# Performance work log

Hardware: AMD Instinct MI355X
Metric: run time of the kernel (lower is better)

## Reference

```python
import jax, jax.numpy as jnp
import numpy as np

N = 24000; E = 384000; NT = 3; IN = 128; HID = 32; ED = 64; NE = 5; FFN = 64; C = 16
HEADS = (8, 8, 1); ALPHA = 0.05; DAL = 2


def _lrelu(x, s):
    return jnp.where(x >= 0, x, s * x)


def _elu(x):
    return jnp.where(x > 0, x, jnp.expm1(x))


def _ln(x, g, b, eps=1e-5):
    m = x.mean(-1, keepdims=True)
    v = ((x - m) ** 2).mean(-1, keepdims=True)
    return (x - m) / jnp.sqrt(v + eps) * g + b


def _l2n(x, eps=1e-12):
    return x / jnp.maximum(jnp.linalg.norm(x, axis=1, keepdims=True), eps)


def _ta(h, src, dst, e_feat, edge_emb, W, We, al, ar, ae, bias, res_W, res_attn, act):
    # SimpleHGN-style heterogeneous graph attention layer (TALayer)
    Hh = al.shape[0]
    feat = (h @ W).reshape(N, Hh, HID)                       # [N,H,D]
    ee = (edge_emb[e_feat] @ We).reshape(E, Hh, ED)          # [E,H,ED]
    el = (feat * al).sum(-1)                                 # [N,H]
    er = (feat * ar).sum(-1)                                 # [N,H]
    lg = _lrelu(el[src] + er[dst] + (ee * ae).sum(-1), 0.2)  # [E,H]
    m = jax.ops.segment_max(lg, dst, num_segments=N)         # edge softmax over dst
    a = jnp.exp(lg - m[dst])
    a = a / jax.ops.segment_sum(a, dst, num_segments=N)[dst]
    if res_attn is not None:
        a = a * (1.0 - ALPHA) + res_attn * ALPHA             # residual attention carry-over
    rst = jax.ops.segment_sum(a[:, :, None] * feat[src], dst, num_segments=N)
    if res_W is not None:
        rst = rst + (h @ res_W).reshape(N, Hh, HID)
    rst = rst + bias
    if act:
        rst = _elu(rst)
    return rst, jax.lax.stop_gradient(a)


def forward(feats, fc_W, fc_b, ntype_emb, W_ntype,
            ta0_edge_emb, ta0_W, ta0_We, ta0_al, ta0_ar, ta0_ae, ta0_bias,
            ta1_edge_emb, ta1_W, ta1_We, ta1_al, ta1_ar, ta1_ae, ta1_bias, ta1_res_W,
            ta2_edge_emb, ta2_W, ta2_We, ta2_al, ta2_ar, ta2_ae, ta2_bias, ta2_res_W,
            da_ln1_g, da_ln1_b, da_Wq, da_bq, da_Wk, da_bk, da_Wv, da_bv, da_Wo, da_bo,
            da_ln2_g, da_ln2_b, da_W1, da_b1, da_W2, da_b2, final_W, logits_W,
            e_feat, node_type, src, dst):
    # per-node-type input projection + leaky_relu(0.01), concat over types -> [N,HID]
    h = _lrelu(jnp.einsum('tni,tio->tno', feats, fc_W) + fc_b[:, None, :], 0.01).reshape(N, HID)
    ntype_feat = (ntype_emb @ W_ntype)[node_type]            # [N,HID]
    h = h * ntype_feat
    h0, a0 = _ta(h, src, dst, e_feat, ta0_edge_emb, ta0_W, ta0_We, ta0_al, ta0_ar, ta0_ae, ta0_bias, None, None, True)
    h = h0.reshape(N, -1)
    h1, _ = _ta(h, src, dst, e_feat, ta1_edge_emb, ta1_W, ta1_We, ta1_al, ta1_ar, ta1_ae, ta1_bias, ta1_res_W, a0, True)
    h = h1.reshape(N, -1)
    hf, _ = _ta(h, src, dst, e_feat, ta2_edge_emb, ta2_W, ta2_We, ta2_al, ta2_ar, ta2_ae, ta2_bias, ta2_res_W, None, False)
    h_feat = hf.reshape(N, HID)
    # dim-wise transformer (DALayer stack): tokens = HID dims, channel = 1
    x = (h_feat * ntype_feat)[:, :, None]                    # [N,HID,1]
    for l in range(DAL):
        y = _ln(x, da_ln1_g[l], da_ln1_b[l])
        q = y @ da_Wq[l] + da_bq[l]
        k = y @ da_Wk[l] + da_bk[l]
        v = y @ da_Wv[l] + da_bv[l]
        att = jax.nn.softmax(jnp.einsum('nqd,nkd->nqk', q, k), axis=-1)  # scale=att_size**-0.5=1
        x = x + (jnp.einsum('nqk,nkd->nqd', att, v) @ da_Wo[l] + da_bo[l])
        y = _ln(x, da_ln2_g[l], da_ln2_b[l])
        x = x + (jax.nn.gelu(y @ da_W1[l] + da_b1[l], approximate=False) @ da_W2[l] + da_b2[l])
    h_dim = _l2n(x[:, :, 0])
    h_final = jnp.concatenate([_l2n(h_feat), h_dim], axis=1) @ final_W
    logits = jax.nn.relu(h_final) @ logits_W
    return logits / jnp.maximum(jnp.linalg.norm(logits, axis=1, keepdims=True), 1e-12)


def setup_inputs():
    key = jax.random.key(0)
    ks = iter(jax.random.split(key, 96))
    def rn(shape, s=0.1):
        return jax.random.normal(next(ks), shape, jnp.float32) * s
    inp = {}
    inp["feats"] = jax.random.normal(next(ks), (NT, N // NT, IN), jnp.float32)
    inp["e_feat"] = jax.random.randint(next(ks), (E,), 0, NE)
    inp["node_type"] = jax.random.randint(next(ks), (N,), 0, NT)
    inp["src"] = jax.random.randint(next(ks), (E,), 0, N)
    inp["dst"] = jax.random.randint(next(ks), (E,), 0, N)
    inp["fc_W"] = rn((NT, IN, HID)); inp["fc_b"] = rn((NT, HID))
    inp["ntype_emb"] = rn((NT, HID)); inp["W_ntype"] = rn((HID, HID))
    ins = (HID, HID * HEADS[0], HID * HEADS[1])
    for l in range(3):
        Hh = HEADS[l]; di = ins[l]; p = "ta%d_" % l
        inp[p + "edge_emb"] = rn((NE, ED))
        inp[p + "W"] = rn((di, Hh * HID))
        inp[p + "We"] = rn((ED, Hh * ED))
        inp[p + "al"] = rn((Hh, HID)); inp[p + "ar"] = rn((Hh, HID)); inp[p + "ae"] = rn((Hh, ED))
        inp[p + "bias"] = jnp.zeros((Hh, HID), jnp.float32)
        if l > 0:
            inp[p + "res_W"] = rn((di, Hh * HID))
    inp["da_ln1_g"] = jnp.ones((DAL, 1), jnp.float32); inp["da_ln1_b"] = jnp.zeros((DAL, 1), jnp.float32)
    inp["da_Wq"] = rn((DAL, 1, 1)); inp["da_bq"] = jnp.zeros((DAL, 1), jnp.float32)
    inp["da_Wk"] = rn((DAL, 1, 1)); inp["da_bk"] = jnp.zeros((DAL, 1), jnp.float32)
    inp["da_Wv"] = rn((DAL, 1, 1)); inp["da_bv"] = jnp.zeros((DAL, 1), jnp.float32)
    inp["da_Wo"] = rn((DAL, 1, 1)); inp["da_bo"] = jnp.zeros((DAL, 1), jnp.float32)
    inp["da_ln2_g"] = jnp.ones((DAL, 1), jnp.float32); inp["da_ln2_b"] = jnp.zeros((DAL, 1), jnp.float32)
    inp["da_W1"] = rn((DAL, 1, FFN)); inp["da_b1"] = jnp.zeros((DAL, FFN), jnp.float32)
    inp["da_W2"] = rn((DAL, FFN, 1)); inp["da_b2"] = jnp.zeros((DAL, 1), jnp.float32)
    inp["final_W"] = rn((2 * HID, HID))
    inp["logits_W"] = rn((HID, C))
    return inp


def reference(feats, fc_W, fc_b, ntype_emb, W_ntype,
              ta0_edge_emb, ta0_W, ta0_We, ta0_al, ta0_ar, ta0_ae, ta0_bias,
              ta1_edge_emb, ta1_W, ta1_We, ta1_al, ta1_ar, ta1_ae, ta1_bias, ta1_res_W,
              ta2_edge_emb, ta2_W, ta2_We, ta2_al, ta2_ar, ta2_ae, ta2_bias, ta2_res_W,
              da_ln1_g, da_ln1_b, da_Wq, da_bq, da_Wk, da_bk, da_Wv, da_bv, da_Wo, da_bo,
              da_ln2_g, da_ln2_b, da_W1, da_b1, da_W2, da_b2, final_W, logits_W,
              e_feat, node_type, src, dst):
    return forward(feats, fc_W, fc_b, ntype_emb, W_ntype,
                   ta0_edge_emb, ta0_W, ta0_We, ta0_al, ta0_ar, ta0_ae, ta0_bias,
                   ta1_edge_emb, ta1_W, ta1_We, ta1_al, ta1_ar, ta1_ae, ta1_bias, ta1_res_W,
                   ta2_edge_emb, ta2_W, ta2_We, ta2_al, ta2_ar, ta2_ae, ta2_bias, ta2_res_W,
                   da_ln1_g, da_ln1_b, da_Wq, da_bq, da_Wk, da_bk, da_Wv, da_bv, da_Wo, da_bo,
                   da_ln2_g, da_ln2_b, da_W1, da_b1, da_W2, da_b2, final_W, logits_W,
                   e_feat, node_type, src, dst)
```

## Files before the change

kernel.cpp:

```cpp
#include <hip/hip_runtime.h>
#include <math.h>

constexpr int kN = 24000;
constexpr int kE = 384000;
constexpr float kAlpha = 0.05f;

typedef unsigned int   u32;
typedef unsigned short u16;
typedef __attribute__((ext_vector_type(8))) short short8;
typedef __attribute__((ext_vector_type(4))) float float4v;

__device__ __forceinline__ float bf2f(u16 x) { return __uint_as_float(((u32)x) << 16); }
__device__ __forceinline__ u16 f2bf(float f) {
  u32 u = __float_as_uint(f);
  return (u16)((u + 0x7fffu + ((u >> 16) & 1u)) >> 16);
}

__global__ void __launch_bounds__(256) zero_ints_kernel(int* __restrict__ p, int n) {
  int i = blockIdx.x * 256 + threadIdx.x;
  if (i < n) p[i] = 0;
}

__global__ void __launch_bounds__(256) count_kernel(const int* __restrict__ dst,
                                                    int* __restrict__ counts) {
  int e = blockIdx.x * 256 + threadIdx.x;
  if (e < kE) atomicAdd(&counts[dst[e]], 1);
}

__global__ void __launch_bounds__(1024) scan_kernel(const int* __restrict__ counts,
                                                    int* __restrict__ row_start) {
  __shared__ int wsum[16];
  __shared__ int carry_s;
  int tid = threadIdx.x, lane = tid & 63, wid = tid >> 6;
  if (tid == 0) { carry_s = 0; row_start[0] = 0; }
  __syncthreads();
  for (int base = 0; base < kN; base += 1024) {
    int x = (base + tid < kN) ? counts[base + tid] : 0;
    #pragma unroll
    for (int off = 1; off < 64; off <<= 1) {
      int y = __shfl_up(x, off);
      if (lane >= off) x += y;
    }
    if (lane == 63) wsum[wid] = x;
    __syncthreads();
    if (tid < 16) {
      int wv = wsum[tid];
      #pragma unroll
      for (int off = 1; off < 16; off <<= 1) {
        int y = __shfl_up(wv, off);
        if (tid >= off) wv += y;
      }
      wsum[tid] = wv;
    }
    __syncthreads();
    int incl = x + carry_s + (wid > 0 ? wsum[wid - 1] : 0);
    if (base + tid < kN) row_start[base + tid + 1] = incl;
    __syncthreads();
    if (tid == 1023) carry_s = incl;
    __syncthreads();
  }
}

__global__ void __launch_bounds__(256) scatter_kernel(const int* __restrict__ dst,
                                                      const int* __restrict__ row_start,
                                                      int* __restrict__ cursor,
                                                      int* __restrict__ edge_ids) {
  int e = blockIdx.x * 256 + threadIdx.x;
  if (e < kE) {
    int n = dst[e];
    int pos = row_start[n] + atomicAdd(&cursor[n], 1);
    edge_ids[pos] = e;
  }
}

__global__ void __launch_bounds__(256) prepack_kernel(
    const float* __restrict__ W0, const float* __restrict__ al0, const float* __restrict__ ar0,
    const float* __restrict__ W1, const float* __restrict__ al1, const float* __restrict__ ar1,
    const float* __restrict__ rW1,
    const float* __restrict__ W2, const float* __restrict__ al2, const float* __restrict__ ar2,
    const float* __restrict__ rW2,
    u16* __restrict__ WT0, u16* __restrict__ WT1, u16* __restrict__ WT2,
    const float* __restrict__ ntype_emb, const float* __restrict__ W_ntype,
    const float* __restrict__ emb0, const float* __restrict__ We0, const float* __restrict__ ae0,
    const float* __restrict__ emb1, const float* __restrict__ We1, const float* __restrict__ ae1,
    const float* __restrict__ emb2, const float* __restrict__ We2, const float* __restrict__ ae2,
    const float* __restrict__ ln1_b, const float* __restrict__ Wv, const float* __restrict__ bv,
    const float* __restrict__ Wo, const float* __restrict__ bo,
    const float* __restrict__ ln2_b, const float* __restrict__ DW1, const float* __restrict__ Db1,
    const float* __restrict__ DW2, const float* __restrict__ Db2,
    float* __restrict__ ntf, float* __restrict__ eterm, float* __restrict__ dadelta) {
  __shared__ float wae[17][64];
  __shared__ float red[128];
  int tid = threadIdx.x;
  if (blockIdx.x < 744) {
    const int SZ0 = 10240, SZ1 = 576 * 256;
    int gid = blockIdx.x * 256 + tid;
    float v = 0.f;
    if (gid < 2048) {
      int n = gid / 32, k = gid % 32;
      if (n < 8)       { for (int d = 0; d < 32; ++d) v += W0[k * 256 + n * 32 + d] * al0[n * 32 + d]; }
      else if (n < 16) { int h = n - 8; for (int d = 0; d < 32; ++d) v += W0[k * 256 + h * 32 + d] * ar0[h * 32 + d]; }
      WT0[n * 32 + k] = f2bf(v);
    } else if (gid < SZ0) {
      int i = gid - 2048;
      int h = i >> 10, rem = i & 1023, d = rem >> 5, k = rem & 31;
      WT0[2048 + i] = f2bf(W0[k * 256 + h * 32 + d]);
    } else if (gid < SZ0 + SZ1) {
      int i = gid - SZ0;
      int n = i / 256, k = i % 256;
      if (n < 256) v = W1[k * 256 + n];
      else if (n < 264) { int h = n - 256; for (int d = 0; d < 32; ++d) v += W1[k * 256 + h * 32 + d] * al1[h * 32 + d]; }
      else if (n < 272) { int h = n - 264; for (int d = 0; d < 32; ++d) v += W1[k * 256 + h * 32 + d] * ar1[h * 32 + d]; }
      else if (n < 528) v = rW1[k * 256 + (n - 272)];
      WT1[n * 256 + k] = f2bf(v);
    } else {
      int i = gid - SZ0 - SZ1;
      int n = i / 256, k = i % 256;
      if (n < 32) v = W2[k * 32 + n];
      else if (n == 32) { for (int d = 0; d < 32; ++d) v += W2[k * 32 + d] * al2[d]; }
      else if (n == 33) { for (int d = 0; d < 32; ++d) v += W2[k * 32 + d] * ar2[d]; }
      else if (n < 66) v = rW2[k * 32 + (n - 34)];
      WT2[n * 256 + k] = f2bf(v);
    }
  } else {
    for (int idx = tid; idx < 17 * 64; idx += 256) {
      int hg = idx >> 6, k = idx & 63;
      const float* We; const float* ae; int Hh, h;
      if (hg < 8)       { We = We0; ae = ae0; Hh = 8; h = hg; }
      else if (hg < 16) { We = We1; ae = ae1; Hh = 8; h = hg - 8; }
      else              { We = We2; ae = ae2; Hh = 1; h = 0; }
      float s = 0.f;
      for (int d = 0; d < 64; ++d) s += We[(size_t)k * Hh * 64 + h * 64 + d] * ae[h * 64 + d];
      wae[hg][k] = s;
    }
    __syncthreads();
    for (int id = tid; id < 85; id += 256) {
      const float* emb; int Hh, t, h, hg, base;
      if (id < 40)      { emb = emb0; Hh = 8; t = id / 8;  h = id % 8; hg = h;      base = 0;  }
      else if (id < 80) { int i = id - 40; emb = emb1; Hh = 8; t = i / 8; h = i % 8; hg = 8 + h; base = 40; }
      else              { int i = id - 80; emb = emb2; Hh = 1; t = i;    h = 0;     hg = 16;    base = 80; }
      float s = 0.f;
      for (int k = 0; k < 64; ++k) s += emb[t * 64 + k] * wae[hg][k];
      eterm[base + t * Hh + h] = s;
    }
    for (int idx = tid; idx < 96; idx += 256) {
      int t = idx / 32, o = idx % 32;
      float s = 0.f;
      for (int k = 0; k < 32; ++k) s += ntype_emb[t * 32 + k] * W_ntype[k * 32 + o];
      ntf[idx] = s;
    }
    for (int i2 = tid; i2 < 128; i2 += 256) {
      int l = i2 >> 6, j = i2 & 63;
      float u = ln2_b[l] * DW1[l * 64 + j] + Db1[l * 64 + j];
      float g = 0.5f * u * (1.0f + erff(u * 0.7071067811865476f));
      red[i2] = g * DW2[l * 64 + j];
    }
    __syncthreads();
    if (tid == 0) {
      float delta = 0.f;
      for (int l = 0; l < 2; ++l) {
        float vs = ln1_b[l] * Wv[l] + bv[l];
        delta += vs * Wo[l] + bo[l] + Db2[l];
      }
      for (int i = 0; i < 128; ++i) delta += red[i];
      *dadelta = delta;
    }
  }
}

__global__ void __launch_bounds__(256) inproj_kernel(
    const float* __restrict__ feats, const float* __restrict__ fc_W,
    const float* __restrict__ fc_b, const float* __restrict__ ntf,
    const int* __restrict__ node_type, u16* __restrict__ hb) {
  int t = blockIdx.x * 256 + threadIdx.x;
  if (t >= kN * 32) return;
  int n = t >> 5, o = t & 31;
  int ty = n / 8000;
  const float* fr = &feats[(size_t)n * 128];
  const float* w  = &fc_W[(size_t)ty * 4096 + o];
  float s = fc_b[ty * 32 + o];
  #pragma unroll
  for (int k = 0; k < 128; k += 4) {
    float4 f = *(const float4*)&fr[k];
    s += f.x * w[(k + 0) * 32] + f.y * w[(k + 1) * 32]
       + f.z * w[(k + 2) * 32] + f.w * w[(k + 3) * 32];
  }
  s = (s < 0.f) ? 0.01f * s : s;
  hb[t] = f2bf(s * ntf[node_type[n] * 32 + o]);
}

template <int K>
__global__ void __launch_bounds__(256) mfma_gemm_kernel(
    const u16* __restrict__ A, const u16* __restrict__ WT,
    const float* __restrict__ bias,
    u16* __restrict__ featb, float* __restrict__ el, float* __restrict__ er,
    u16* __restrict__ resb, float* __restrict__ resf,
    int NT, int N1, int HH, int N2) {
  constexpr int RB = K * 2;
  constexpr int CPR = K / 8;
  __shared__ __align__(16) u16 As[64 * K];
  __shared__ __align__(16) u16 Bs[64 * K];
  const int tid = threadIdx.x;
  const int l = tid & 63;
  const int w = tid >> 6;
  const int wm = w >> 1, wn = w & 1;
  const int m0 = blockIdx.x * 64;
  const int kslot = l >> 4;
  const int l15 = l & 15;

  #pragma unroll
  for (int c = tid; c < 64 * CPR; c += 256) {
    int row = c / CPR, ch = c - row * CPR;
    int off = (row * RB + ch * 16) ^ ((row & 7) << 4);
    *(uint4*)((char*)As + off) = *(const uint4*)(A + (size_t)(m0 + row) * K + ch * 8);
  }

  for (int ct = 0; ct < NT; ++ct) {
    __syncthreads();
    #pragma unroll
    for (int c = tid; c < 64 * CPR; c += 256) {
      int row = c / CPR, ch = c - row * CPR;
      int off = (row * RB + ch * 16) ^ ((row & 7) << 4);
      *(uint4*)((char*)Bs + off) = *(const uint4*)(WT + (size_t)(ct * 64 + row) * K + ch * 8);
    }
    __syncthreads();

    float4v acc[2][2];
    #pragma unroll
    for (int f = 0; f < 2; ++f)
      #pragma unroll
      for (int g = 0; g < 2; ++g) { acc[f][g][0]=0.f; acc[f][g][1]=0.f; acc[f][g][2]=0.f; acc[f][g][3]=0.f; }

    #pragma unroll
    for (int kc = 0; kc < K; kc += 32) {
      short8 af[2], bf[2];
      #pragma unroll
      for (int f = 0; f < 2; ++f) {
        int row = wm * 32 + f * 16 + l15;
        int off = (row * RB + kc * 2 + kslot * 16) ^ ((row & 7) << 4);
        af[f] = *(const short8*)((const char*)As + off);
      }
      #pragma unroll
      for (int g = 0; g < 2; ++g) {
        int n = wn * 32 + g * 16 + l15;
        int off = (n * RB + kc * 2 + kslot * 16) ^ ((n & 7) << 4);
        bf[g] = *(const short8*)((const char*)Bs + off);
      }
      #pragma unroll
      for (int f = 0; f < 2; ++f)
        #pragma unroll
        for (int g = 0; g < 2; ++g)
          acc[f][g] = __builtin_amdgcn_mfma_f32_16x16x32_bf16(af[f], bf[g], acc[f][g], 0, 0, 0);
    }

    const int rbase = kslot * 4;
    #pragma unroll
    for (int f = 0; f < 2; ++f) {
      #pragma unroll
      for (int g = 0; g < 2; ++g) {
        int gc = ct * 64 + wn * 32 + g * 16 + l15;
        #pragma unroll
        for (int reg = 0; reg < 4; ++reg) {
          int gr = m0 + wm * 32 + f * 16 + rbase + reg;
          float v = acc[f][g][reg];
          if (gc < N1) {
            featb[(size_t)gr * N1 + gc] = f2bf(v);
          } else if (gc < N1 + HH) {
            el[(size_t)gr * HH + (gc - N1)] = v;
          } else if (gc < N1 + 2 * HH) {
            er[(size_t)gr * HH + (gc - N1 - HH)] = v;
          } else if (gc < N1 + 2 * HH + N2) {
            int c2 = gc - N1 - 2 * HH;
            float vv = v + bias[c2];
            if (resb) resb[(size_t)gr * N2 + c2] = f2bf(vv);
            else      resf[(size_t)gr * N2 + c2] = vv;
          }
        }
      }
    }
  }
}

__global__ void __launch_bounds__(256) agg8h_kernel(
    const int* __restrict__ row_start, const int* __restrict__ edge_ids,
    const int* __restrict__ src, const int* __restrict__ ef,
    const float* __restrict__ el, const float* __restrict__ er,
    const float* __restrict__ eterm,
    const u16* __restrict__ Hb,
    _Float16* __restrict__ a0h,
    u16* __restrict__ Gb) {
  int n = (blockIdx.x * 256 + threadIdx.x) >> 6;
  if (n >= kN) return;
  int l = threadIdx.x & 63;
  int h = l >> 3, s = l & 7;
  int s0 = row_start[n], s1 = row_start[n + 1];
  float ern = er[n * 8 + h];
  float et0 = eterm[0 * 8 + h], et1 = eterm[1 * 8 + h], et2 = eterm[2 * 8 + h];
  float et3 = eterm[3 * 8 + h], et4 = eterm[4 * 8 + h];
  float m = -1e30f, ssum = 0.f;
  for (int i = s0 + s; i < s1; i += 8) {
    int e = edge_ids[i];
    int efc = ef[e];
    float etv = (efc == 0) ? et0 : (efc == 1) ? et1 : (efc == 2) ? et2 : (efc == 3) ? et3 : et4;
    float lg = el[src[e] * 8 + h] + ern + etv;
    lg = (lg < 0.f) ? 0.2f * lg : lg;
    if (lg > m) { ssum = ssum * expf(m - lg) + 1.f; m = lg; }
    else        { ssum += expf(lg - m); }
  }
  #pragma unroll
  for (int mk = 1; mk <= 4; mk <<= 1) {
    float om = __shfl_xor(m, mk);
    float os = __shfl_xor(ssum, mk);
    float nm = fmaxf(m, om);
    ssum = ssum * expf(m - nm) + os * expf(om - nm);
    m = nm;
  }
  float inv = 1.f / ssum;
  float4 acc = make_float4(0.f, 0.f, 0.f, 0.f);
  int i = s0;
  for (; i + 8 <= s1; i += 8) {
    int e = edge_ids[i + s];
    int sek = src[e];
    int efc = ef[e];
    float etv = (efc == 0) ? et0 : (efc == 1) ? et1 : (efc == 2) ? et2 : (efc == 3) ? et3 : et4;
    float lg = el[sek * 8 + h] + ern + etv;
    lg = (lg < 0.f) ? 0.2f * lg : lg;
    float am = expf(lg - m) * inv;
    a0h[(size_t)e * 8 + h] = (_Float16)am;
    #pragma unroll
    for (int j = 0; j < 8; ++j) {
      float aj = __shfl(am, (h << 3) + j);
      int sej = __shfl(sek, j);
      ushort4 fv = *(const ushort4*)(Hb + (size_t)sej * 32 + s * 4);
      acc.x = fmaf(aj, bf2f(fv.x), acc.x);
      acc.y = fmaf(aj, bf2f(fv.y), acc.y);
      acc.z = fmaf(aj, bf2f(fv.z), acc.z);
      acc.w = fmaf(aj, bf2f(fv.w), acc.w);
    }
  }
  if (i < s1) {
    int cnt = s1 - i;
    float am = 0.f; int sek = 0;
    if (s < cnt) {
      int e = edge_ids[i + s];
      sek = src[e];
      int efc = ef[e];
      float etv = (efc == 0) ? et0 : (efc == 1) ? et1 : (efc == 2) ? et2 : (efc == 3) ? et3 : et4;
      float lg = el[sek * 8 + h] + ern + etv;
      lg = (lg < 0.f) ? 0.2f * lg : lg;
      am = expf(lg - m) * inv;
      a0h[(size_t)e * 8 + h] = (_Float16)am;
    }
    for (int j = 0; j < cnt; ++j) {
      float aj = __shfl(am, (h << 3) + j);
      int sej = __shfl(sek, j);
      ushort4 fv = *(const ushort4*)(Hb + (size_t)sej * 32 + s * 4);
      acc.x = fmaf(aj, bf2f(fv.x), acc.x);
      acc.y = fmaf(aj, bf2f(fv.y), acc.y);
      acc.z = fmaf(aj, bf2f(fv.z), acc.z);
      acc.w = fmaf(aj, bf2f(fv.w), acc.w);
    }
  }
  ushort4 pw;
  pw.x = f2bf(acc.x); pw.y = f2bf(acc.y); pw.z = f2bf(acc.z); pw.w = f2bf(acc.w);
  *(ushort4*)(Gb + (size_t)n * 256 + h * 32 + s * 4) = pw;
}

__global__ void __launch_bounds__(256) bd_gemm_kernel(
    const u16* __restrict__ Gb,
    const u16* __restrict__ WbdT,
    const float* __restrict__ bias,
    u16* __restrict__ outb) {
  __shared__ __align__(16) u16 As[64 * 256];
  __shared__ __align__(16) u16 Bs[8 * 32 * 32];
  const int tid = threadIdx.x;
  const int l = tid & 63;
  const int w = tid >> 6;
  const int m0 = blockIdx.x * 64;
  const int kslot = l >> 4, l15 = l & 15;
  for (int c = tid; c < 64 * 32; c += 256) {
    int row = c >> 5, ch = c & 31;
    int off = (row * 512 + ch * 16) ^ ((row & 7) << 4);
    *(uint4*)((char*)As + off) = *(const uint4*)(Gb + (size_t)(m0 + row) * 256 + ch * 8);
  }
  for (int c = tid; c < 256 * 4; c += 256) {
    int r = c >> 2, ch = c & 3;
    int off = (r * 64 + ch * 16) ^ ((r & 7) << 4);
    *(uint4*)((char*)Bs + off) = *(const uint4*)(WbdT + (size_t)r * 32 + ch * 8);
  }
  __syncthreads();
  #pragma unroll
  for (int hh = 0; hh < 2; ++hh) {
    int h = w * 2 + hh;
    short8 af[4];
    #pragma unroll
    for (int f = 0; f < 4; ++f) {
      int row = f * 16 + l15;
      int off = (row * 512 + h * 64 + kslot * 16) ^ ((row & 7) << 4);
      af[f] = *(const short8*)((const char*)As + off);
    }
    short8 bf[2];
    #pragma unroll
    for (int g = 0; g < 2; ++g) {
      int r = h * 32 + g * 16 + l15;
      int off = (r * 64 + kslot * 16) ^ ((r & 7) << 4);
      bf[g] = *(const short8*)((const char*)Bs + off);
    }
    #pragma unroll
    for (int f = 0; f < 4; ++f) {
      #pragma unroll
      for (int g = 0; g < 2; ++g) {
        float4v acc = {0.f, 0.f, 0.f, 0.f};
        acc = __builtin_amdgcn_mfma_f32_16x16x32_bf16(af[f], bf[g], acc, 0, 0, 0);
        #pragma unroll
        for (int reg = 0; reg < 4; ++reg) {
          int gr = m0 + f * 16 + kslot * 4 + reg;
          int gc = h * 32 + g * 16 + l15;
          float v = acc[reg] + bias[gc];
          v = (v > 0.f) ? v : expm1f(v);
          outb[(size_t)gr * 256 + gc] = f2bf(v);
        }
      }
    }
  }
}

__global__ void __launch_bounds__(256) agg8w_kernel(
    const int* __restrict__ row_start, const int* __restrict__ edge_ids,
    const int* __restrict__ src, const int* __restrict__ ef,
    const float* __restrict__ el, const float* __restrict__ er,
    const float* __restrict__ eterm,
    const u16* __restrict__ featb,
    const _Float16* __restrict__ a0h,
    const u16* __restrict__ accb,
    u16* __restrict__ outb) {
  int n = (blockIdx.x * 256 + threadIdx.x) >> 6;
  if (n >= kN) return;
  int l = threadIdx.x & 63;
  int h = l >> 3, s = l & 7;
  int s0 = row_start[n], s1 = row_start[n + 1];
  float ern = er[n * 8 + h];
  float et0 = eterm[0 * 8 + h], et1 = eterm[1 * 8 + h], et2 = eterm[2 * 8 + h];
  float et3 = eterm[3 * 8 + h], et4 = eterm[4 * 8 + h];
  float m = -1e30f, ssum = 0.f;
  for (int i = s0 + s; i < s1; i += 8) {
    int e = edge_ids[i];
    int efc = ef[e];
    float etv = (efc == 0) ? et0 : (efc == 1) ? et1 : (efc == 2) ? et2 : (efc == 3) ? et3 : et4;
    float lg = el[src[e] * 8 + h] + ern + etv;
    lg = (lg < 0.f) ? 0.2f * lg : lg;
    if (lg > m) { ssum = ssum * expf(m - lg) + 1.f; m = lg; }
    else        { ssum += expf(lg - m); }
  }
  #pragma unroll
  for (int mk = 1; mk <= 4; mk <<= 1) {
    float om = __shfl_xor(m, mk);
    float os = __shfl_xor(ssum, mk);
    float nm = fmaxf(m, om);
    ssum = ssum * expf(m - nm) + os * expf(om - nm);
    m = nm;
  }
  float inv = 1.f / ssum;
  const size_t rowoff = (size_t)n * 256 + h * 32 + s * 4;
  ushort4 rv = *(const ushort4*)(accb + rowoff);
  float4 acc = make_float4(bf2f(rv.x), bf2f(rv.y), bf2f(rv.z), bf2f(rv.w));
  int i = s0;
  for (; i + 8 <= s1; i += 8) {
    int e = edge_ids[i + s];
    int sek = src[e];
    int efc = ef[e];
    float etv = (efc == 0) ? et0 : (efc == 1) ? et1 : (efc == 2) ? et2 : (efc == 3) ? et3 : et4;
    float lg = el[sek * 8 + h] + ern + etv;
    lg = (lg < 0.f) ? 0.2f * lg : lg;
    float am = expf(lg - m) * inv;
    am = am * (1.f - kAlpha) + (float)a0h[(size_t)e * 8 + h] * kAlpha;
    #pragma unroll
    for (int j = 0; j < 8; ++j) {
      float aj = __shfl(am, (h << 3) + j);
      int sej = __shfl(sek, j);
      ushort4 fv = *(const ushort4*)(featb + (size_t)sej * 256 + h * 32 + s * 4);
      acc.x = fmaf(aj, bf2f(fv.x), acc.x);
      acc.y = fmaf(aj, bf2f(fv.y), acc.y);
      acc.z = fmaf(aj, bf2f(fv.z), acc.z);
      acc.w = fmaf(aj, bf2f(fv.w), acc.w);
    }
  }
  if (i < s1) {
    int cnt = s1 - i;
    float am = 0.f; int sek = 0;
    if (s < cnt) {
      int e = edge_ids[i + s];
      sek = src[e];
      int efc = ef[e];
      float etv = (efc == 0) ? et0 : (efc == 1) ? et1 : (efc == 2) ? et2 : (efc == 3) ? et3 : et4;
      float lg = el[sek * 8 + h] + ern + etv;
      lg = (lg < 0.f) ? 0.2f * lg : lg;
      am = expf(lg - m) * inv;
      am = am * (1.f - kAlpha) + (float)a0h[(size_t)e * 8 + h] * kAlpha;
    }
    for (int j = 0; j < cnt; ++j) {
      float aj = __shfl(am, (h << 3) + j);
      int sej = __shfl(sek, j);
      ushort4 fv = *(const ushort4*)(featb + (size_t)sej * 256 + h * 32 + s * 4);
      acc.x = fmaf(aj, bf2f(fv.x), acc.x);
      acc.y = fmaf(aj, bf2f(fv.y), acc.y);
      acc.z = fmaf(aj, bf2f(fv.z), acc.z);
      acc.w = fmaf(aj, bf2f(fv.w), acc.w);
    }
  }
  acc.x = (acc.x > 0.f) ? acc.x : expm1f(acc.x);
  acc.y = (acc.y > 0.f) ? acc.y : expm1f(acc.y);
  acc.z = (acc.z > 0.f) ? acc.z : expm1f(acc.z);
  acc.w = (acc.w > 0.f) ? acc.w : expm1f(acc.w);
  ushort4 pw;
  pw.x = f2bf(acc.x); pw.y = f2bf(acc.y); pw.z = f2bf(acc.z); pw.w = f2bf(acc.w);
  *(ushort4*)(outb + rowoff) = pw;
}

__global__ void __launch_bounds__(256) aggw1_final_kernel(
    const int* __restrict__ row_start, const int* __restrict__ edge_ids,
    const int* __restrict__ src, const int* __restrict__ ef,
    const float* __restrict__ el, const float* __restrict__ er,
    const float* __restrict__ eterm,
    const u16* __restrict__ featb,
    const float* __restrict__ S2,
    const float* __restrict__ ntf, const int* __restrict__ node_type,
    const float* __restrict__ dadelta,
    const float* __restrict__ finalW, const float* __restrict__ logitsW,
    float* __restrict__ out) {
  __shared__ float fWs[2048];
  __shared__ float lWs[512];
  __shared__ float abuf[8][32];
  __shared__ float bbuf[8][32];
  __shared__ float sbuf[8][32];
  const int tid = threadIdx.x;
  for (int i = tid; i < 2048; i += 256) fWs[i] = finalW[i];
  for (int i = tid; i < 512; i += 256) lWs[i] = logitsW[i];
  const int slot = tid >> 5;
  const int g = tid & 31;
  const int gb = tid & 32;
  const int n = blockIdx.x * 8 + slot;
  const int s0 = row_start[n], s1 = row_start[n + 1];
  float ern = er[n];
  float et0 = eterm[0], et1 = eterm[1], et2 = eterm[2], et3 = eterm[3], et4 = eterm[4];
  float m = -1e30f, ssum = 0.f;
  for (int i = s0 + g; i < s1; i += 32) {
    int e = edge_ids[i];
    int efc = ef[e];
    float etv = (efc == 0) ? et0 : (efc == 1) ? et1 : (efc == 2) ? et2 : (efc == 3) ? et3 : et4;
    float lg = el[src[e]] + ern + etv;
    lg = (lg < 0.f) ? 0.2f * lg : lg;
    if (lg > m) { ssum = ssum * expf(m - lg) + 1.f; m = lg; }
    else        { ssum += expf(lg - m); }
  }
  #pragma unroll
  for (int mk = 1; mk <= 16; mk <<= 1) {
    float om = __shfl_xor(m, mk);
    float os = __shfl_xor(ssum, mk);
    float nm = fmaxf(m, om);
    ssum = ssum * expf(m - nm) + os * expf(om - nm);
    m = nm;
  }
  float inv = 1.f / ssum;
  float acc = S2[(size_t)n * 32 + g];
  int i = s0;
  for (; i + 32 <= s1; i += 32) {
    int e = edge_ids[i + g];
    int sek = src[e];
    int efc = ef[e];
    float etv = (efc == 0) ? et0 : (efc == 1) ? et1 : (efc == 2) ? et2 : (efc == 3) ? et3 : et4;
    float lg = el[sek] + ern + etv;
    lg = (lg < 0.f) ? 0.2f * lg : lg;
    float am = expf(lg - m) * inv;
    #pragma unroll
    for (int j = 0; j < 32; ++j) {
      float aj = __shfl(am, gb + j);
      int sej = __shfl(sek, gb + j);
      acc = fmaf(aj, bf2f(featb[(size_t)sej * 32 + g]), acc);
    }
  }
  if (i < s1) {
    int cnt = s1 - i;
    float am = 0.f; int sek = 0;
    if (g < cnt) {
      int e = edge_ids[i + g];
      sek = src[e];
      int efc = ef[e];
      float etv = (efc == 0) ? et0 : (efc == 1) ? et1 : (efc == 2) ? et2 : (efc == 3) ? et3 : et4;
      float lg = el[sek] + ern + etv;
      lg = (lg < 0.f) ? 0.2f * lg : lg;
      am = expf(lg - m) * inv;
    }
    for (int j = 0; j < cnt; ++j) {
      float aj = __shfl(am, gb + j);
      int sej = __shfl(sek, gb + j);
      acc = fmaf(aj, bf2f(featb[(size_t)sej * 32 + g]), acc);
    }
  }
  float delta = dadelta[0];
  float ntv = ntf[node_type[n] * 32 + g];
  float av = acc;
  float bv = acc * ntv + delta;
  float na = av * av, nb = bv * bv;
  #pragma unroll
  for (int mk = 1; mk <= 16; mk <<= 1) {
    na += __shfl_xor(na, mk);
    nb += __shfl_xor(nb, mk);
  }
  float inva = 1.f / fmaxf(sqrtf(na), 1e-12f);
  float invb = 1.f / fmaxf(sqrtf(nb), 1e-12f);
  __syncthreads();
  abuf[slot][g] = av * inva;
  bbuf[slot][g] = bv * invb;
  __syncthreads();
  float s = 0.f;
  #pragma unroll
  for (int d = 0; d < 32; ++d)
    s += abuf[slot][d] * fWs[d * 32 + g] + bbuf[slot][d] * fWs[(32 + d) * 32 + g];
  s = fmaxf(s, 0.f);
  sbuf[slot][g] = s;
  __syncthreads();
  if (g < 16) {
    float lg = 0.f;
    #pragma unroll
    for (int o = 0; o < 32; ++o) lg += sbuf[slot][o] * lWs[o * 16 + g];
    float nl = lg * lg;
    #pragma unroll
    for (int mk = 1; mk <= 8; mk <<= 1) nl += __shfl_xor(nl, mk);
    float invl = 1.f / fmaxf(sqrtf(nl), 1e-12f);
    out[(size_t)n * 16 + g] = lg * invl;
  }
}

extern "C" void kernel_launch(void* const* d_in, const int* in_sizes, int n_in,
                              void* d_out, int out_size, void* d_ws, size_t ws_size,
                              hipStream_t stream) {
  const float* feats     = (const float*)d_in[0];
  const int*   e_feat    = (const int*)d_in[1];
  const int*   node_type = (const int*)d_in[2];
  const int*   src       = (const int*)d_in[3];
  const int*   dst       = (const int*)d_in[4];
  const float* fc_W      = (const float*)d_in[5];
  const float* fc_b      = (const float*)d_in[6];
  const float* ntype_emb = (const float*)d_in[7];
  const float* W_ntype   = (const float*)d_in[8];
  const float* ta_edge_emb[3] = {(const float*)d_in[9],  (const float*)d_in[16], (const float*)d_in[24]};
  const float* ta_W[3]        = {(const float*)d_in[10], (const float*)d_in[17], (const float*)d_in[25]};
  const float* ta_We[3]       = {(const float*)d_in[11], (const float*)d_in[18], (const float*)d_in[26]};
  const float* ta_al[3]       = {(const float*)d_in[12], (const float*)d_in[19], (const float*)d_in[27]};
  const float* ta_ar[3]       = {(const float*)d_in[13], (const float*)d_in[20], (const float*)d_in[28]};
  const float* ta_ae[3]       = {(const float*)d_in[14], (const float*)d_in[21], (const float*)d_in[29]};
  const float* ta_bias[3]     = {(const float*)d_in[15], (const float*)d_in[22], (const float*)d_in[30]};
  const float* ta1_res_W = (const float*)d_in[23];
  const float* ta2_res_W = (const float*)d_in[31];
  const float* da_ln1_b  = (const float*)d_in[33];
  const float* da_Wv     = (const float*)d_in[38];
  const float* da_bv     = (const float*)d_in[39];
  const float* da_Wo     = (const float*)d_in[40];
  const float* da_bo     = (const float*)d_in[41];
  const float* da_ln2_b  = (const float*)d_in[43];
  const float* da_W1     = (const float*)d_in[44];
  const float* da_b1     = (const float*)d_in[45];
  const float* da_W2     = (const float*)d_in[46];
  const float* da_b2     = (const float*)d_in[47];
  const float* final_W   = (const float*)d_in[48];
  const float* logits_W  = (const float*)d_in[49];
  float* out = (float*)d_out;

  char* base = (char*)d_ws;
  int* iws       = (int*)base;
  int* counts    = iws;
  int* cursor    = iws + kN;
  int* row_start = iws + 2 * kN;
  int* edge_ids  = iws + 2 * kN + kN + 1;
  char* p = base + (size_t)456004 * 4;
  float* ntf = (float*)p;                     p += 512;
  float* etm = (float*)p;                     p += 512;
  float* dad = (float*)p;                     p += 64;
  float* el  = (float*)p;                     p += (size_t)kN * 8 * 4;
  float* er  = (float*)p;                     p += (size_t)kN * 8 * 4;
  float* S2  = (float*)p;                     p += (size_t)kN * 32 * 4;
  u16*   Hb  = (u16*)p;                       p += (size_t)kN * 32 * 2;
  _Float16* a0h = (_Float16*)p;               p += (size_t)kE * 8 * 2;
  u16* featb = (u16*)p;                       p += (size_t)kN * 256 * 2;
  u16* Rb0   = (u16*)p;                       p += (size_t)kN * 256 * 2;
  u16* Rpr   = (u16*)p;                       p += (size_t)kN * 256 * 2;
  u16* WT0   = (u16*)p;                       p += (size_t)320 * 32 * 2;
  u16* WT1   = (u16*)p;                       p += (size_t)576 * 256 * 2;
  u16* WT2   = (u16*)p;                       p += (size_t)128 * 256 * 2;
  u16* WT0el = WT0;
  u16* Wbd0T = WT0 + 2048;

  zero_ints_kernel<<<(2 * kN + 255) / 256, 256, 0, stream>>>(counts, 2 * kN);
  count_kernel<<<kE / 256, 256, 0, stream>>>(dst, counts);
  scan_kernel<<<1, 1024, 0, stream>>>(counts, row_start);
  scatter_kernel<<<kE / 256, 256, 0, stream>>>(dst, row_start, cursor, edge_ids);

  prepack_kernel<<<745, 256, 0, stream>>>(
      ta_W[0], ta_al[0], ta_ar[0],
      ta_W[1], ta_al[1], ta_ar[1], ta1_res_W,
      ta_W[2], ta_al[2], ta_ar[2], ta2_res_W,
      WT0, WT1, WT2,
      ntype_emb, W_ntype,
      ta_edge_emb[0], ta_We[0], ta_ae[0],
      ta_edge_emb[1], ta_We[1], ta_ae[1],
      ta_edge_emb[2], ta_We[2], ta_ae[2],
      da_ln1_b, da_Wv, da_bv, da_Wo, da_bo,
      da_ln2_b, da_W1, da_b1, da_W2, da_b2,
      ntf, etm, dad);

  inproj_kernel<<<(kN * 32) / 256, 256, 0, stream>>>(feats, fc_W, fc_b, ntf, node_type, Hb);

  mfma_gemm_kernel<32><<<kN / 64, 256, 0, stream>>>(
      Hb, WT0el, nullptr, nullptr, el, er, nullptr, nullptr, 1, 0, 8, 0);
  agg8h_kernel<<<kN / 4, 256, 0, stream>>>(
      row_start, edge_ids, src, e_feat, el, er, etm, Hb, a0h, featb);
  bd_gemm_kernel<<<kN / 64, 256, 0, stream>>>(featb, Wbd0T, ta_bias[0], Rb0);

  mfma_gemm_kernel<256><<<kN / 64, 256, 0, stream>>>(
      Rb0, WT1, ta_bias[1], featb, el, er, Rpr, nullptr, 9, 256, 8, 256);
  agg8w_kernel<<<kN / 4, 256, 0, stream>>>(
      row_start, edge_ids, src, e_feat, el, er, etm + 40, featb, a0h, Rpr, Rpr);

  mfma_gemm_kernel<256><<<kN / 64, 256, 0, stream>>>(
      Rpr, WT2, ta_bias[2], featb, el, er, nullptr, S2, 2, 32, 1, 32);
  aggw1_final_kernel<<<kN / 8, 256, 0, stream>>>(
      row_start, edge_ids, src, e_feat, el, er, etm + 80, featb, S2,
      ntf, node_type, dad, final_W, logits_W, out);
}
```

Measured before the change: 490.0 us.

## Use head-major slab layouts, split GEMM column tiles across blocks, parallel CSR alloc

```diff
diff --git a/kernel.cpp b/kernel.cpp
--- a/kernel.cpp
+++ b/kernel.cpp
@@ -27,38 +27,23 @@
   if (e < kE) atomicAdd(&counts[dst[e]], 1);
 }
 
-__global__ void __launch_bounds__(1024) scan_kernel(const int* __restrict__ counts,
+__global__ void __launch_bounds__(256) alloc_kernel(const int* __restrict__ counts,
+                                                    int* __restrict__ gcur,
                                                     int* __restrict__ row_start) {
-  __shared__ int wsum[16];
-  __shared__ int carry_s;
-  int tid = threadIdx.x, lane = tid & 63, wid = tid >> 6;
-  if (tid == 0) { carry_s = 0; row_start[0] = 0; }
-  __syncthreads();
-  for (int base = 0; base < kN; base += 1024) {
-    int x = (base + tid < kN) ? counts[base + tid] : 0;
-    #pragma unroll
-    for (int off = 1; off < 64; off <<= 1) {
-      int y = __shfl_up(x, off);
-      if (lane >= off) x += y;
-    }
-    if (lane == 63) wsum[wid] = x;
-    __syncthreads();
-    if (tid < 16) {
-      int wv = wsum[tid];
-      #pragma unroll
-      for (int off = 1; off < 16; off <<= 1) {
-        int y = __shfl_up(wv, off);
-        if (tid >= off) wv += y;
-      }
-      wsum[tid] = wv;
-    }
-    __syncthreads();
-    int incl = x + carry_s + (wid > 0 ? wsum[wid - 1] : 0);
-    if (base + tid < kN) row_start[base + tid + 1] = incl;
-    __syncthreads();
-    if (tid == 1023) carry_s = incl;
-    __syncthreads();
-  }
+  int t = blockIdx.x * 256 + threadIdx.x;
+  int lane = threadIdx.x & 63;
+  int c = (t < kN) ? counts[t] : 0;
+  int x = c;
+  #pragma unroll
+  for (int off = 1; off < 64; off <<= 1) {
+    int y = __shfl_up(x, off);
+    if (lane >= off) x += y;
+  }
+  int wtotal = __shfl(x, 63);
+  int base = 0;
+  if (lane == 63) base = atomicAdd(gcur, wtotal);
+  base = __shfl(base, 63);
+  if (t < kN) row_start[t] = base + x - c;
 }
 
 __global__ void __launch_bounds__(256) scatter_kernel(const int* __restrict__ dst,
@@ -189,13 +174,13 @@
   hb[t] = f2bf(s * ntf[node_type[n] * 32 + o]);
 }
 
-template <int K>
+template <int K, bool SLAB>
 __global__ void __launch_bounds__(256) mfma_gemm_kernel(
     const u16* __restrict__ A, const u16* __restrict__ WT,
     const float* __restrict__ bias,
     u16* __restrict__ featb, float* __restrict__ el, float* __restrict__ er,
     u16* __restrict__ resb, float* __restrict__ resf,
-    int NT, int N1, int HH, int N2) {
+    int tpb, int N1, int HH, int N2) {
   constexpr int RB = K * 2;
   constexpr int CPR = K / 8;
   __shared__ __align__(16) u16 As[64 * K];
@@ -204,7 +189,7 @@
   const int l = tid & 63;
   const int w = tid >> 6;
   const int wm = w >> 1, wn = w & 1;
-  const int m0 = blockIdx.x * 64;
+  const int m0 = blockIdx.y * 64;
   const int kslot = l >> 4;
   const int l15 = l & 15;
 
@@ -215,7 +200,8 @@
     *(uint4*)((char*)As + off) = *(const uint4*)(A + (size_t)(m0 + row) * K + ch * 8);
   }
 
-  for (int ct = 0; ct < NT; ++ct) {
+  for (int t = 0; t < tpb; ++t) {
+    int ct = blockIdx.x * tpb + t;
     __syncthreads();
     #pragma unroll
     for (int c = tid; c < 64 * CPR; c += 256) {
@@ -264,11 +250,14 @@
           int gr = m0 + wm * 32 + f * 16 + rbase + reg;
           float v = acc[f][g][reg];
           if (gc < N1) {
-            featb[(size_t)gr * N1 + gc] = f2bf(v);
+            if (SLAB) featb[((size_t)(gc >> 5) * kN + gr) * 32 + (gc & 31)] = f2bf(v);
+            else      featb[(size_t)gr * N1 + gc] = f2bf(v);
           } else if (gc < N1 + HH) {
-            el[(size_t)gr * HH + (gc - N1)] = v;
+            if (SLAB) el[(size_t)(gc - N1) * kN + gr] = v;
+            else      el[(size_t)gr * HH + (gc - N1)] = v;
           } else if (gc < N1 + 2 * HH) {
-            er[(size_t)gr * HH + (gc - N1 - HH)] = v;
+            if (SLAB) er[(size_t)(gc - N1 - HH) * kN + gr] = v;
+            else      er[(size_t)gr * HH + (gc - N1 - HH)] = v;
           } else if (gc < N1 + 2 * HH + N2) {
             int c2 = gc - N1 - 2 * HH;
             float vv = v + bias[c2];
@@ -282,18 +271,19 @@
 }
 
 __global__ void __launch_bounds__(256) agg8h_kernel(
-    const int* __restrict__ row_start, const int* __restrict__ edge_ids,
+    const int* __restrict__ row_start, const int* __restrict__ counts,
+    const int* __restrict__ edge_ids,
     const int* __restrict__ src, const int* __restrict__ ef,
     const float* __restrict__ el, const float* __restrict__ er,
     const float* __restrict__ eterm,
     const u16* __restrict__ Hb,
-    _Float16* __restrict__ a0h,
+    _Float16* __restrict__ a0s,
     u16* __restrict__ Gb) {
   int n = (blockIdx.x * 256 + threadIdx.x) >> 6;
   if (n >= kN) return;
   int l = threadIdx.x & 63;
   int h = l >> 3, s = l & 7;
-  int s0 = row_start[n], s1 = row_start[n + 1];
+  int s0 = row_start[n], s1 = s0 + counts[n];
   float ern = er[n * 8 + h];
   float et0 = eterm[0 * 8 + h], et1 = eterm[1 * 8 + h], et2 = eterm[2 * 8 + h];
   float et3 = eterm[3 * 8 + h], et4 = eterm[4 * 8 + h];
@@ -326,7 +316,7 @@
     float lg = el[sek * 8 + h] + ern + etv;
     lg = (lg < 0.f) ? 0.2f * lg : lg;
     float am = expf(lg - m) * inv;
-    a0h[(size_t)e * 8 + h] = (_Float16)am;
+    a0s[(size_t)h * kE + e] = (_Float16)am;
     #pragma unroll
     for (int j = 0; j < 8; ++j) {
       float aj = __shfl(am, (h << 3) + j);
@@ -349,7 +339,7 @@
       float lg = el[sek * 8 + h] + ern + etv;
       lg = (lg < 0.f) ? 0.2f * lg : lg;
       am = expf(lg - m) * inv;
-      a0h[(size_t)e * 8 + h] = (_Float16)am;
+      a0s[(size_t)h * kE + e] = (_Float16)am;
     }
     for (int j = 0; j < cnt; ++j) {
       float aj = __shfl(am, (h << 3) + j);
@@ -367,10 +357,8 @@
 }
 
 __global__ void __launch_bounds__(256) bd_gemm_kernel(
-    const u16* __restrict__ Gb,
-    const u16* __restrict__ WbdT,
-    const float* __restrict__ bias,
-    u16* __restrict__ outb) {
+    const u16* __restrict__ Gb, const u16* __restrict__ WbdT,
+    const float* __restrict__ bias, u16* __restrict__ outb) {
   __shared__ __align__(16) u16 As[64 * 256];
   __shared__ __align__(16) u16 Bs[8 * 32 * 32];
   const int tid = threadIdx.x;
@@ -425,29 +413,37 @@
   }
 }
 
-__global__ void __launch_bounds__(256) agg8w_kernel(
-    const int* __restrict__ row_start, const int* __restrict__ edge_ids,
+__global__ void __launch_bounds__(256) agg8s_kernel(
+    const int* __restrict__ row_start, const int* __restrict__ counts,
+    const int* __restrict__ edge_ids,
     const int* __restrict__ src, const int* __restrict__ ef,
-    const float* __restrict__ el, const float* __restrict__ er,
+    const float* __restrict__ el_s,
+    const float* __restrict__ er_s,
     const float* __restrict__ eterm,
-    const u16* __restrict__ featb,
-    const _Float16* __restrict__ a0h,
+    const u16* __restrict__ feat_s,
+    const _Float16* __restrict__ a0s,
     const u16* __restrict__ accb,
     u16* __restrict__ outb) {
-  int n = (blockIdx.x * 256 + threadIdx.x) >> 6;
-  if (n >= kN) return;
-  int l = threadIdx.x & 63;
-  int h = l >> 3, s = l & 7;
-  int s0 = row_start[n], s1 = row_start[n + 1];
-  float ern = er[n * 8 + h];
-  float et0 = eterm[0 * 8 + h], et1 = eterm[1 * 8 + h], et2 = eterm[2 * 8 + h];
-  float et3 = eterm[3 * 8 + h], et4 = eterm[4 * 8 + h];
+  const int hd = blockIdx.x & 7;
+  const int chunk = blockIdx.x >> 3;
+  const int tid = threadIdx.x;
+  const int slot = tid >> 3;
+  const int g = tid & 7;
+  const int n = chunk * 32 + slot;
+  const int lbase = (tid & 63) & ~7;
+  int s0 = row_start[n], s1 = s0 + counts[n];
+  const float* el_h = el_s + (size_t)hd * kN;
+  const u16* feat_h = feat_s + (size_t)hd * kN * 32;
+  const _Float16* a0_h = a0s + (size_t)hd * kE;
+  float ern = er_s[(size_t)hd * kN + n];
+  float et0 = eterm[0 * 8 + hd], et1 = eterm[1 * 8 + hd], et2 = eterm[2 * 8 + hd];
+  float et3 = eterm[3 * 8 + hd], et4 = eterm[4 * 8 + hd];
   float m = -1e30f, ssum = 0.f;
-  for (int i = s0 + s; i < s1; i += 8) {
+  for (int i = s0 + g; i < s1; i += 8) {
     int e = edge_ids[i];
     int efc = ef[e];
     float etv = (efc == 0) ? et0 : (efc == 1) ? et1 : (efc == 2) ? et2 : (efc == 3) ? et3 : et4;
-    float lg = el[src[e] * 8 + h] + ern + etv;
+    float lg = el_h[src[e]] + ern + etv;
     lg = (lg < 0.f) ? 0.2f * lg : lg;
     if (lg > m) { ssum = ssum * expf(m - lg) + 1.f; m = lg; }
     else        { ssum += expf(lg - m); }
@@ -461,24 +457,24 @@
     m = nm;
   }
   float inv = 1.f / ssum;
-  const size_t rowoff = (size_t)n * 256 + h * 32 + s * 4;
+  const size_t rowoff = (size_t)n * 256 + hd * 32 + g * 4;
   ushort4 rv = *(const ushort4*)(accb + rowoff);
   float4 acc = make_float4(bf2f(rv.x), bf2f(rv.y), bf2f(rv.z), bf2f(rv.w));
   int i = s0;
   for (; i + 8 <= s1; i += 8) {
-    int e = edge_ids[i + s];
+    int e = edge_ids[i + g];
     int sek = src[e];
     int efc = ef[e];
     float etv = (efc == 0) ? et0 : (efc == 1) ? et1 : (efc == 2) ? et2 : (efc == 3) ? et3 : et4;
-    float lg = el[sek * 8 + h] + ern + etv;
+    float lg = el_h[sek] + ern + etv;
     lg = (lg < 0.f) ? 0.2f * lg : lg;
     float am = expf(lg - m) * inv;
-    am = am * (1.f - kAlpha) + (float)a0h[(size_t)e * 8 + h] * kAlpha;
+    am = am * (1.f - kAlpha) + (float)a0_h[e] * kAlpha;
     #pragma unroll
     for (int j = 0; j < 8; ++j) {
-      float aj = __shfl(am, (h << 3) + j);
-      int sej = __shfl(sek, j);
-      ushort4 fv = *(const ushort4*)(featb + (size_t)sej * 256 + h * 32 + s * 4);
+      float aj = __shfl(am, lbase + j);
+      int sej = __shfl(sek, lbase + j);
+      ushort4 fv = *(const ushort4*)(feat_h + (size_t)sej * 32 + g * 4);
       acc.x = fmaf(aj, bf2f(fv.x), acc.x);
       acc.y = fmaf(aj, bf2f(fv.y), acc.y);
       acc.z = fmaf(aj, bf2f(fv.z), acc.z);
@@ -488,20 +484,20 @@
   if (i < s1) {
     int cnt = s1 - i;
     float am = 0.f; int sek = 0;
-    if (s < cnt) {
-      int e = edge_ids[i + s];
+    if (g < cnt) {
+      int e = edge_ids[i + g];
       sek = src[e];
       int efc = ef[e];
       float etv = (efc == 0) ? et0 : (efc == 1) ? et1 : (efc == 2) ? et2 : (efc == 3) ? et3 : et4;
-      float lg = el[sek * 8 + h] + ern + etv;
+      float lg = el_h[sek] + ern + etv;
       lg = (lg < 0.f) ? 0.2f * lg : lg;
       am = expf(lg - m) * inv;
-      am = am * (1.f - kAlpha) + (float)a0h[(size_t)e * 8 + h] * kAlpha;
+      am = am * (1.f - kAlpha) + (float)a0_h[e] * kAlpha;
     }
     for (int j = 0; j < cnt; ++j) {
-      float aj = __shfl(am, (h << 3) + j);
-      int sej = __shfl(sek, j);
-      ushort4 fv = *(const ushort4*)(featb + (size_t)sej * 256 + h * 32 + s * 4);
+      float aj = __shfl(am, lbase + j);
+      int sej = __shfl(sek, lbase + j);
+      ushort4 fv = *(const ushort4*)(feat_h + (size_t)sej * 32 + g * 4);
       acc.x = fmaf(aj, bf2f(fv.x), acc.x);
       acc.y = fmaf(aj, bf2f(fv.y), acc.y);
       acc.z = fmaf(aj, bf2f(fv.z), acc.z);
@@ -518,7 +514,8 @@
 }
 
 __global__ void __launch_bounds__(256) aggw1_final_kernel(
-    const int* __restrict__ row_start, const int* __restrict__ edge_ids,
+    const int* __restrict__ row_start, const int* __restrict__ counts,
+    const int* __restrict__ edge_ids,
     const int* __restrict__ src, const int* __restrict__ ef,
     const float* __restrict__ el, const float* __restrict__ er,
     const float* __restrict__ eterm,
@@ -540,7 +537,7 @@
   const int g = tid & 31;
   const int gb = tid & 32;
   const int n = blockIdx.x * 8 + slot;
-  const int s0 = row_start[n], s1 = row_start[n + 1];
+  const int s0 = row_start[n], s1 = s0 + counts[n];
   float ern = er[n];
   float et0 = eterm[0], et1 = eterm[1], et2 = eterm[2], et3 = eterm[3], et4 = eterm[4];
   float m = -1e30f, ssum = 0.f;
@@ -671,8 +668,9 @@
   int* iws       = (int*)base;
   int* counts    = iws;
   int* cursor    = iws + kN;
-  int* row_start = iws + 2 * kN;
-  int* edge_ids  = iws + 2 * kN + kN + 1;
+  int* gcur      = iws + 2 * kN;
+  int* row_start = iws + 2 * kN + 4;
+  int* edge_ids  = iws + 3 * kN + 4;
   char* p = base + (size_t)456004 * 4;
   float* ntf = (float*)p;                     p += 512;
   float* etm = (float*)p;                     p += 512;
@@ -681,7 +679,7 @@
   float* er  = (float*)p;                     p += (size_t)kN * 8 * 4;
   float* S2  = (float*)p;                     p += (size_t)kN * 32 * 4;
   u16*   Hb  = (u16*)p;                       p += (size_t)kN * 32 * 2;
-  _Float16* a0h = (_Float16*)p;               p += (size_t)kE * 8 * 2;
+  _Float16* a0s = (_Float16*)p;               p += (size_t)kE * 8 * 2;
   u16* featb = (u16*)p;                       p += (size_t)kN * 256 * 2;
   u16* Rb0   = (u16*)p;                       p += (size_t)kN * 256 * 2;
   u16* Rpr   = (u16*)p;                       p += (size_t)kN * 256 * 2;
@@ -691,9 +689,9 @@
   u16* WT0el = WT0;
   u16* Wbd0T = WT0 + 2048;
 
-  zero_ints_kernel<<<(2 * kN + 255) / 256, 256, 0, stream>>>(counts, 2 * kN);
+  zero_ints_kernel<<<(2 * kN + 4 + 255) / 256, 256, 0, stream>>>(counts, 2 * kN + 4);
   count_kernel<<<kE / 256, 256, 0, stream>>>(dst, counts);
-  scan_kernel<<<1, 1024, 0, stream>>>(counts, row_start);
+  alloc_kernel<<<(kN + 255) / 256, 256, 0, stream>>>(counts, gcur, row_start);
   scatter_kernel<<<kE / 256, 256, 0, stream>>>(dst, row_start, cursor, edge_ids);
 
   prepack_kernel<<<745, 256, 0, stream>>>(
@@ -711,20 +709,21 @@
 
   inproj_kernel<<<(kN * 32) / 256, 256, 0, stream>>>(feats, fc_W, fc_b, ntf, node_type, Hb);
 
-  mfma_gemm_kernel<32><<<kN / 64, 256, 0, stream>>>(
+  mfma_gemm_kernel<32, false><<<dim3(1, kN / 64), 256, 0, stream>>>(
       Hb, WT0el, nullptr, nullptr, el, er, nullptr, nullptr, 1, 0, 8, 0);
   agg8h_kernel<<<kN / 4, 256, 0, stream>>>(
-      row_start, edge_ids, src, e_feat, el, er, etm, Hb, a0h, featb);
+      row_start, counts, edge_ids, src, e_feat, el, er, etm, Hb, a0s, featb);
   bd_gemm_kernel<<<kN / 64, 256, 0, stream>>>(featb, Wbd0T, ta_bias[0], Rb0);
 
-  mfma_gemm_kernel<256><<<kN / 64, 256, 0, stream>>>(
-      Rb0, WT1, ta_bias[1], featb, el, er, Rpr, nullptr, 9, 256, 8, 256);
-  agg8w_kernel<<<kN / 4, 256, 0, stream>>>(
-      row_start, edge_ids, src, e_feat, el, er, etm + 40, featb, a0h, Rpr, Rpr);
-
-  mfma_gemm_kernel<256><<<kN / 64, 256, 0, stream>>>(
-      Rpr, WT2, ta_bias[2], featb, el, er, nullptr, S2, 2, 32, 1, 32);
+  mfma_gemm_kernel<256, true><<<dim3(3, kN / 64), 256, 0, stream>>>(
+      Rb0, WT1, ta_bias[1], featb, el, er, Rpr, nullptr, 3, 256, 8, 256);
+  agg8s_kernel<<<(kN / 32) * 8, 256, 0, stream>>>(
+      row_start, counts, edge_ids, src, e_feat, el, er, etm + 40,
+      featb, a0s, Rpr, Rpr);
+
+  mfma_gemm_kernel<256, false><<<dim3(2, kN / 64), 256, 0, stream>>>(
+      Rpr, WT2, ta_bias[2], featb, el, er, nullptr, S2, 1, 32, 1, 32);
   aggw1_final_kernel<<<kN / 8, 256, 0, stream>>>(
-      row_start, edge_ids, src, e_feat, el, er, etm + 80, featb, S2,
+      row_start, counts, edge_ids, src, e_feat, el, er, etm + 80, featb, S2,
       ntf, node_type, dad, final_W, logits_W, out);
 }
```

Measured after the change: 587.1 us. 1.2x slower.
